# Performance work log

Hardware: AMD Instinct MI355X
Metric: run time of the kernel (lower is better)

## Reference

```python
import jax, jax.numpy as jnp
import numpy as np

M, N = 4096, 4096


def _makhoul_perm(n):
    # Makhoul even/odd reordering: v[k] = x[2k] for k < ceil(n/2),
    # v[n-1-k] = x[2k+1] for the rest. This is the same input permutation
    # the dct2_fft2 kernel applies before its rfft2.
    idx = np.empty(n, dtype=np.int32)
    half = (n + 1) // 2
    idx[:half] = 2 * np.arange(half)
    idx[half:] = 2 * (n - 1 - np.arange(half, n)) + 1
    return jnp.asarray(idx)


def _dct2_1d_last(x):
    # Unnormalized DCT-II along the last axis via a same-length FFT plus
    # twiddle (expk) multiply:  C[k] = Re( exp(-i*pi*k/(2n)) * FFT(v)[k] )
    # which equals sum_m x[m] * cos(pi*k*(2m+1)/(2n)).
    n = x.shape[-1]
    v = jnp.take(x, _makhoul_perm(n), axis=-1)
    V = jnp.fft.fft(v, axis=-1)
    k = jnp.arange(n)
    expk = jnp.exp((-1j * np.pi / (2.0 * n)) * k)  # twiddle factors (expkM/expkN)
    return jnp.real(V * expk).astype(x.dtype)


def setup_inputs() -> dict:
    key = jax.random.key(0)
    x = jax.random.normal(key, (M, N), dtype=jnp.float32)
    return {"x": x}


def reference(x):
    # Separable 2D DCT-II: along axis -1 (uses expkN), then axis -2 (expkM).
    y = _dct2_1d_last(x)        # DCT over columns index (length N)
    y = _dct2_1d_last(y.T).T    # DCT over rows index (length M)
    return y
```

## Files before the change

### kernel.cpp

```cpp
#include <hip/hip_runtime.h>
#include <hip/hip_fp16.h>
#include <stdint.h>


#define NF 4096

__device__ __forceinline__ int physi(int e) { return e ^ ((e >> 4) & 15); }

__device__ __forceinline__ int cfi(int n, int c) {
    return (n << 2) | (c ^ (((n >> 2) ^ (n >> 4)) & 3));
}

__device__ __forceinline__ float2 cadd(float2 a, float2 b) {
    float2 r; r.x = a.x + b.x; r.y = a.y + b.y; return r;
}
__device__ __forceinline__ float2 csub(float2 a, float2 b) {
    float2 r; r.x = a.x - b.x; r.y = a.y - b.y; return r;
}
__device__ __forceinline__ float2 cmulc(float2 a, float2 b) {
    float2 r; r.x = a.x * b.x - a.y * b.y; r.y = a.x * b.y + a.y * b.x; return r;
}
__device__ __forceinline__ float2 rotm(float2 a) {
    float2 r; r.x = a.y; r.y = -a.x; return r;
}

__global__ __launch_bounds__(256) void setup_tables(float* __restrict__ tw,
                                                    float* __restrict__ ek) {
    int idx = blockIdx.x * 256 + threadIdx.x;
    if (idx < 4416) {
        int p, u; float denom;
        if (idx < 64)       { p = idx >> 3;         u = idx & 7;  denom = 64.0f; }
        else if (idx < 320) { int r = idx - 64;  p = r >> 4; u = r & 15; denom = 256.0f; }
        else                { int r = idx - 320; p = r >> 4; u = r & 15; denom = 4096.0f; }
        float phi = (float)(p * u) * (6.283185307179586f / denom);
        float s, c; __sincosf(phi, &s, &c);
        tw[2 * idx]     = c;
        tw[2 * idx + 1] = -s;
    } else if (idx < 8512) {
        int k = idx - 4416;
        float th = (float)k * (3.141592653589793f / 8192.0f);
        float s, c; __sincosf(th, &s, &c);
        ek[2 * k]     = c;
        ek[2 * k + 1] = s;
    }
}

#define RADIX8(Xv, E0, E1, E2, E3, O0, g1, g2, g3)                             \
    float2 t0 = cadd(Xv[0], Xv[4]), t1 = csub(Xv[0], Xv[4]);                   \
    float2 t2 = cadd(Xv[2], Xv[6]), t3 = csub(Xv[2], Xv[6]);                   \
    float2 E0 = cadd(t0, t2), E2 = csub(t0, t2);                               \
    float2 r3 = rotm(t3);                                                      \
    float2 E1 = cadd(t1, r3), E3 = csub(t1, r3);                               \
    float2 s0 = cadd(Xv[1], Xv[5]), s1 = csub(Xv[1], Xv[5]);                   \
    float2 s2 = cadd(Xv[3], Xv[7]), s3 = csub(Xv[3], Xv[7]);                   \
    float2 O0 = cadd(s0, s2), O2 = csub(s0, s2);                               \
    float2 r7 = rotm(s3);                                                      \
    float2 O1 = cadd(s1, r7), O3 = csub(s1, r7);                               \
    const float SQ = 0.7071067811865476f;                                      \
    float2 g1; g1.x = SQ * (O1.x + O1.y); g1.y = SQ * (O1.y - O1.x);           \
    float2 g2 = rotm(O2);                                                      \
    float2 g3; g3.x = SQ * (O3.y - O3.x); g3.y = -SQ * (O3.x + O3.y);

#define RADIX8_OUT(Xv, Ov)                                                     \
    {                                                                          \
        RADIX8(Xv, E0, E1, E2, E3, O0, g1, g2, g3)                             \
        Ov[0] = cadd(E0, O0); Ov[1] = cadd(E1, g1);                            \
        Ov[2] = cadd(E2, g2); Ov[3] = cadd(E3, g3);                            \
        Ov[4] = csub(E0, O0); Ov[5] = csub(E1, g1);                            \
        Ov[6] = csub(E2, g2); Ov[7] = csub(E3, g3);                            \
    }

__device__ __forceinline__ void dft16(float2* x) {
    float2 E[8], O[8];
    {
        float2 a[8];
        #pragma unroll
        for (int m = 0; m < 8; ++m) a[m] = x[2 * m];
        RADIX8_OUT(a, E)
    }
    {
        float2 a[8];
        #pragma unroll
        for (int m = 0; m < 8; ++m) a[m] = x[2 * m + 1];
        RADIX8_OUT(a, O)
    }
    const float2 W1 = { 0.9238795325112867f, -0.3826834323650898f};
    const float2 W2 = { 0.7071067811865476f, -0.7071067811865476f};
    const float2 W3 = { 0.3826834323650898f, -0.9238795325112867f};
    const float2 W5 = {-0.3826834323650898f, -0.9238795325112867f};
    const float2 W6 = {-0.7071067811865476f, -0.7071067811865476f};
    const float2 W7 = {-0.9238795325112867f, -0.3826834323650898f};
    float2 t;
    x[0] = cadd(E[0], O[0]);  x[8]  = csub(E[0], O[0]);
    t = cmulc(O[1], W1); x[1] = cadd(E[1], t); x[9]  = csub(E[1], t);
    t = cmulc(O[2], W2); x[2] = cadd(E[2], t); x[10] = csub(E[2], t);
    t = cmulc(O[3], W3); x[3] = cadd(E[3], t); x[11] = csub(E[3], t);
    t = rotm(O[4]);      x[4] = cadd(E[4], t); x[12] = csub(E[4], t);
    t = cmulc(O[5], W5); x[5] = cadd(E[5], t); x[13] = csub(E[5], t);
    t = cmulc(O[6], W6); x[6] = cadd(E[6], t); x[14] = csub(E[6], t);
    t = cmulc(O[7], W7); x[7] = cadd(E[7], t); x[15] = csub(E[7], t);
}

__global__ __launch_bounds__(256) void dct_rows(const float* __restrict__ In,
                                                __half* __restrict__ Out,
                                                const float* __restrict__ tw,
                                                const float* __restrict__ ek) {
    __shared__ float2 buf[NF];
    const int j = threadIdx.x;
    const int b = blockIdx.x;
    const float* in0 = In + (size_t)(2 * b) * NF;
    const float* in1 = in0 + NF;
    __half* out0 = Out + (size_t)b * NF;
    __half* out1 = Out + (size_t)(4095 - b) * NF;

    const float4* i40 = (const float4*)in0;
    const float4* i41 = (const float4*)in1;
    #pragma unroll
    for (int c = 0; c < 4; ++c) {
        float4 a0 = i40[j + 256 * c];
        float4 a1 = i41[j + 256 * c];
        int nb = 2 * j + 512 * c;
        float2 z0; z0.x = a0.x; z0.y = a1.x;
        float2 z1; z1.x = a0.z; z1.y = a1.z;
        float2 z2; z2.x = a0.y; z2.y = a1.y;
        float2 z3; z3.x = a0.w; z3.y = a1.w;
        buf[physi(nb)]        = z0;
        buf[physi(nb + 1)]    = z1;
        buf[physi(4095 - nb)] = z2;
        buf[physi(4094 - nb)] = z3;
    }
    __syncthreads();

    float2 x[16];

    #pragma unroll
    for (int k = 0; k < 16; ++k)
        x[k] = buf[physi(j + 256 * k)];
    dft16(x);
    __syncthreads();
    #pragma unroll
    for (int i = 0; i < 16; ++i)
        buf[physi(16 * j + i)] = x[i];
    __syncthreads();

    {
        const int p = j & 15, q = j >> 4;
        #pragma unroll
        for (int k = 0; k < 16; ++k)
            x[k] = buf[physi(j + 256 * k)];
        const float2* twp = (const float2*)tw + 64 + p * 16;
        #pragma unroll
        for (int k = 1; k < 16; ++k)
            x[k] = cmulc(x[k], twp[k]);
        dft16(x);
        __syncthreads();
        int wb = p + 256 * q;
        #pragma unroll
        for (int i = 0; i < 16; ++i)
            buf[physi(wb + 16 * i)] = x[i];
        __syncthreads();
    }

    {
        #pragma unroll
        for (int k = 0; k < 16; ++k)
            x[k] = buf[physi(j + 256 * k)];
        const float2* twp = (const float2*)tw + 320 + j * 16;
        #pragma unroll
        for (int k = 1; k < 16; ++k)
            x[k] = cmulc(x[k], twp[k]);
        dft16(x);
        #pragma unroll
        for (int i = 0; i < 16; ++i)
            buf[physi(j + 256 * i)] = x[i];
    }
    __syncthreads();

    #pragma unroll
    for (int i = 0; i < 16; ++i) {
        int k = j + 256 * i;
        int m = (NF - k) & (NF - 1);
        float2 Zk = x[i];
        float2 Zm = buf[physi(m)];
        float2 E = ((const float2*)ek)[k];
        out0[k] = __float2half(0.5f * ((Zk.x + Zm.x) * E.x + (Zk.y - Zm.y) * E.y));
        out1[k] = __float2half(0.5f * ((Zk.y + Zm.y) * E.x - (Zk.x - Zm.x) * E.y));
    }
}

__global__ __launch_bounds__(1024) void col_dct(const __half* __restrict__ V,
                                                float* __restrict__ Out,
                                                const float* __restrict__ tw,
                                                const float* __restrict__ ek) {
    extern __shared__ float2 buf[];
    const int t = threadIdx.x;
    const int bi = blockIdx.x;
    const int ct = (bi & 7) * 64 + (bi >> 3);
    const int c = t & 3;
    const int j = t >> 2;

    {
        const int h = t & 1, r0 = t >> 1;
        #pragma unroll
        for (int k = 0; k < 8; ++k) {
            int r = r0 + 512 * k;
            uint2 v = *(const uint2*)(V + (size_t)r * NF + 8 * ct + 4 * h);
            float2 a = __half22float2(*(__half2*)&v.x);
            float2 d = __half22float2(*(__half2*)&v.y);
            buf[cfi(r, 2 * h)]     = a;
            buf[cfi(r, 2 * h + 1)] = d;
        }
    }
    __syncthreads();

    float2 x[16];

    #pragma unroll
    for (int k = 0; k < 16; ++k)
        x[k] = buf[cfi(j + 256 * k, c)];
    dft16(x);
    __syncthreads();
    #pragma unroll
    for (int i = 0; i < 16; ++i)
        buf[cfi(16 * j + i, c)] = x[i];
    __syncthreads();

    {
        const int p = j & 15, q = j >> 4;
        #pragma unroll
        for (int k = 0; k < 16; ++k)
            x[k] = buf[cfi(j + 256 * k, c)];
        const float2* twp = (const float2*)tw + 64 + p * 16;
        #pragma unroll
        for (int k = 1; k < 16; ++k)
            x[k] = cmulc(x[k], twp[k]);
        dft16(x);
        __syncthreads();
        int wb = p + 256 * q;
        #pragma unroll
        for (int i = 0; i < 16; ++i)
            buf[cfi(wb + 16 * i, c)] = x[i];
        __syncthreads();
    }

    {
        #pragma unroll
        for (int k = 0; k < 16; ++k)
            x[k] = buf[cfi(j + 256 * k, c)];
        const float2* twp = (const float2*)tw + 320 + j * 16;
        #pragma unroll
        for (int k = 1; k < 16; ++k)
            x[k] = cmulc(x[k], twp[k]);
        dft16(x);
        #pragma unroll
        for (int i = 0; i < 16; ++i)
            buf[cfi(j + 256 * i, c)] = x[i];
    }
    __syncthreads();

    float* base = Out + 8 * (size_t)ct;
    #pragma unroll
    for (int i = 0; i < 16; ++i) {
        int k = j + 256 * i;
        int m = (NF - k) & (NF - 1);
        float2 Zk = x[i];
        float2 Zm = buf[cfi(m, c)];
        float2 E = ((const float2*)ek)[k];
        float2 r;
        r.x = 0.5f * ((Zk.x + Zm.x) * E.x + (Zk.y - Zm.y) * E.y);
        r.y = 0.5f * ((Zk.y + Zm.y) * E.x - (Zk.x - Zm.x) * E.y);
        *(float2*)&base[(size_t)k * NF + 2 * c] = r;
    }
}

extern "C" void kernel_launch(void* const* d_in, const int* in_sizes, int n_in,
                              void* d_out, int out_size, void* d_ws, size_t ws_size,
                              hipStream_t stream) {
    const float* x = (const float*)d_in[0];
    float* out = (float*)d_out;

    float* tw = (float*)d_ws;
    float* ek = tw + 8832;
    __half* V = (__half*)(ek + 8192);
    if (ws_size < (size_t)68096 + (size_t)NF * NF * sizeof(__half)) return;

    static bool attr_done = false;
    if (!attr_done) {
        (void)hipFuncSetAttribute((const void*)col_dct,
                                  hipFuncAttributeMaxDynamicSharedMemorySize,
                                  131072);
        attr_done = true;
    }

    setup_tables<<<34, 256, 0, stream>>>(tw, ek);
    dct_rows<<<NF / 2, 256, 0, stream>>>(x, V, tw, ek);
    col_dct<<<512, 1024, 131072, stream>>>(V, out, tw, ek);
}
```

Before: 161.4 us.

## Halve column-DCT block width to two complex columns per block with padded LDS

The column FFT kernel now handles 2 complex columns (4 half values) per block with 512 threads instead of 4 columns with 1024 threads. This doubles the grid to 1024 blocks and roughly halves shared memory per block (about 68 KB instead of 128 KB), so more than one block can fit on a CU. The XOR swizzle for shared-memory indexing is replaced by a padded layout (one extra slot every 8 rows) to avoid bank conflicts. In exchange, global reads and writes per row become narrower (8-byte loads, 16-byte column strips), which may reduce coalescing efficiency.

```diff
diff --git a/kernel.cpp b/kernel.cpp
--- a/kernel.cpp
+++ b/kernel.cpp
@@ -7,8 +7,8 @@
 
 __device__ __forceinline__ int physi(int e) { return e ^ ((e >> 4) & 15); }
 
-__device__ __forceinline__ int cfi(int n, int c) {
-    return (n << 2) | (c ^ (((n >> 2) ^ (n >> 4)) & 3));
+__device__ __forceinline__ int cfi2(int n, int c) {
+    return 2 * n + c + (n >> 3);
 }
 
 __device__ __forceinline__ float2 cadd(float2 a, float2 b) {
@@ -188,28 +188,23 @@
     }
 }
 
-__global__ __launch_bounds__(1024) void col_dct(const __half* __restrict__ V,
+__global__ __launch_bounds__(512) void col_dct2(const __half* __restrict__ V,
                                                 float* __restrict__ Out,
                                                 const float* __restrict__ tw,
                                                 const float* __restrict__ ek) {
     extern __shared__ float2 buf[];
     const int t = threadIdx.x;
     const int bi = blockIdx.x;
-    const int ct = (bi & 7) * 64 + (bi >> 3);
-    const int c = t & 3;
-    const int j = t >> 2;
-
-    {
-        const int h = t & 1, r0 = t >> 1;
-        #pragma unroll
-        for (int k = 0; k < 8; ++k) {
-            int r = r0 + 512 * k;
-            uint2 v = *(const uint2*)(V + (size_t)r * NF + 8 * ct + 4 * h);
-            float2 a = __half22float2(*(__half2*)&v.x);
-            float2 d = __half22float2(*(__half2*)&v.y);
-            buf[cfi(r, 2 * h)]     = a;
-            buf[cfi(r, 2 * h + 1)] = d;
-        }
+    const int ct = (bi & 7) * 128 + (bi >> 3);
+    const int c = t & 1;
+    const int j = t >> 1;
+
+    #pragma unroll
+    for (int k = 0; k < 8; ++k) {
+        int r = t + 512 * k;
+        uint2 v = *(const uint2*)(V + (size_t)r * NF + 4 * ct);
+        buf[cfi2(r, 0)] = __half22float2(*(__half2*)&v.x);
+        buf[cfi2(r, 1)] = __half22float2(*(__half2*)&v.y);
     }
     __syncthreads();
 
@@ -217,19 +212,19 @@
 
     #pragma unroll
     for (int k = 0; k < 16; ++k)
-        x[k] = buf[cfi(j + 256 * k, c)];
+        x[k] = buf[cfi2(j + 256 * k, c)];
     dft16(x);
     __syncthreads();
     #pragma unroll
     for (int i = 0; i < 16; ++i)
-        buf[cfi(16 * j + i, c)] = x[i];
+        buf[cfi2(16 * j + i, c)] = x[i];
     __syncthreads();
 
     {
         const int p = j & 15, q = j >> 4;
         #pragma unroll
         for (int k = 0; k < 16; ++k)
-            x[k] = buf[cfi(j + 256 * k, c)];
+            x[k] = buf[cfi2(j + 256 * k, c)];
         const float2* twp = (const float2*)tw + 64 + p * 16;
         #pragma unroll
         for (int k = 1; k < 16; ++k)
@@ -239,14 +234,14 @@
         int wb = p + 256 * q;
         #pragma unroll
         for (int i = 0; i < 16; ++i)
-            buf[cfi(wb + 16 * i, c)] = x[i];
-        __syncthreads();
-    }
-
-    {
-        #pragma unroll
-        for (int k = 0; k < 16; ++k)
-            x[k] = buf[cfi(j + 256 * k, c)];
+            buf[cfi2(wb + 16 * i, c)] = x[i];
+        __syncthreads();
+    }
+
+    {
+        #pragma unroll
+        for (int k = 0; k < 16; ++k)
+            x[k] = buf[cfi2(j + 256 * k, c)];
         const float2* twp = (const float2*)tw + 320 + j * 16;
         #pragma unroll
         for (int k = 1; k < 16; ++k)
@@ -254,17 +249,17 @@
         dft16(x);
         #pragma unroll
         for (int i = 0; i < 16; ++i)
-            buf[cfi(j + 256 * i, c)] = x[i];
-    }
-    __syncthreads();
-
-    float* base = Out + 8 * (size_t)ct;
+            buf[cfi2(j + 256 * i, c)] = x[i];
+    }
+    __syncthreads();
+
+    float* base = Out + 4 * (size_t)ct;
     #pragma unroll
     for (int i = 0; i < 16; ++i) {
         int k = j + 256 * i;
         int m = (NF - k) & (NF - 1);
         float2 Zk = x[i];
-        float2 Zm = buf[cfi(m, c)];
+        float2 Zm = buf[cfi2(m, c)];
         float2 E = ((const float2*)ek)[k];
         float2 r;
         r.x = 0.5f * ((Zk.x + Zm.x) * E.x + (Zk.y - Zm.y) * E.y);
@@ -286,13 +281,13 @@
 
     static bool attr_done = false;
     if (!attr_done) {
-        (void)hipFuncSetAttribute((const void*)col_dct,
+        (void)hipFuncSetAttribute((const void*)col_dct2,
                                   hipFuncAttributeMaxDynamicSharedMemorySize,
-                                  131072);
+                                  69632);
         attr_done = true;
     }
 
     setup_tables<<<34, 256, 0, stream>>>(tw, ek);
     dct_rows<<<NF / 2, 256, 0, stream>>>(x, V, tw, ek);
-    col_dct<<<512, 1024, 131072, stream>>>(V, out, tw, ek);
-}
+    col_dct2<<<1024, 512, 69632, stream>>>(V, out, tw, ek);
+}
```

Result: slower. 170.1 us (+5.4%).
